# Kernel tuning notes

Measured on AMD Instinct MI355X. Metric: run time of the kernel, lower is better.

## Reference

```python
import jax, jax.numpy as jnp
import numpy as np
import math

BS, QL, KL = 2, 2048, 2048
H, D = 16, 64          # n_heads, cell_dim
QS = KS = VS = 1024    # query/key/value feature sizes
HD = H * D


def setup_inputs() -> dict:
    key = jax.random.key(0)
    ks = jax.random.split(key, 12)
    s_in = 1.0 / math.sqrt(QS)
    s_hd = 1.0 / math.sqrt(HD)
    return {
        "query": jax.random.normal(ks[0], (BS, QL, QS), jnp.float32),
        "key": jax.random.normal(ks[1], (BS, KL, KS), jnp.float32),
        "value": jax.random.normal(ks[2], (BS, KL, VS), jnp.float32),
        # nn.Linear weights stored as [in, out] for x @ W + b
        "Wq_w": jax.random.normal(ks[3], (QS, HD), jnp.float32) * s_in,
        "Wq_b": jax.random.normal(ks[4], (HD,), jnp.float32) * s_in,
        "Wk_w": jax.random.normal(ks[5], (KS, HD), jnp.float32) * s_in,
        "Wk_b": jax.random.normal(ks[6], (HD,), jnp.float32) * s_in,
        "Wv_w": jax.random.normal(ks[7], (VS, HD), jnp.float32) * s_in,
        "Wv_b": jax.random.normal(ks[8], (HD,), jnp.float32) * s_in,
        "Wo_w": jax.random.normal(ks[9], (HD, HD), jnp.float32) * s_hd,
        "Wo_b": jax.random.normal(ks[10], (HD,), jnp.float32) * s_hd,
    }


def reference(query, key, value, Wq_w, Wq_b, Wk_w, Wk_b, Wv_w, Wv_b, Wo_w, Wo_b):
    bs, ql, _ = query.shape
    kl = key.shape[1]
    # project and split heads; torch .chunk along dim 2 == head-major reshape
    q = (query @ Wq_w + Wq_b).reshape(bs, ql, H, D).transpose(0, 2, 1, 3)  # bhqd
    k = (key @ Wk_w + Wk_b).reshape(bs, kl, H, D).transpose(0, 2, 1, 3)    # bhkd
    v = (value @ Wv_w + Wv_b).reshape(bs, kl, H, D).transpose(0, 2, 1, 3)  # bhkd
    scores = jnp.einsum("bhqd,bhkd->bhqk", q, k) / jnp.sqrt(jnp.float32(D))
    # log_softmax(...).exp() == softmax (use_mask=False path)
    w = jax.nn.softmax(scores, axis=-1)
    heads = jnp.einsum("bhqk,bhkd->bhqd", w, v)
    out = heads.transpose(0, 2, 1, 3).reshape(bs, ql, HD)  # concat heads on dim 2
    return out @ Wo_w + Wo_b
```

## Files before the change

### kernel.cpp

```cpp
#include <hip/hip_runtime.h>

#define BSZ 2
#define SEQ 2048
#define NH 16
#define DHD 64
#define HDIM 1024
#define FS 1024
#define MR (BSZ*SEQ)
#define L2E 1.4426950408889634f

typedef __bf16 bf16x8 __attribute__((ext_vector_type(8)));
typedef __bf16 bf16x2t __attribute__((ext_vector_type(2)));
typedef float f32x4 __attribute__((ext_vector_type(4)));
typedef float f32x16 __attribute__((ext_vector_type(16)));
typedef unsigned short u16;
typedef unsigned int u32;

__device__ __forceinline__ u16 f2bf(float f) {
  u32 x = __float_as_uint(f);
  return (u16)((x + 0x7fffu + ((x >> 16) & 1u)) >> 16);
}

__device__ __forceinline__ u32 pack2bf(float a, float b) {
  bf16x2t t = {(__bf16)a, (__bf16)b};
  return __builtin_bit_cast(u32, t);
}

__device__ __forceinline__ void gload16(const void* g, void* l) {
  __builtin_amdgcn_global_load_lds(
      (const __attribute__((address_space(1))) u32*)g,
      (__attribute__((address_space(3))) u32*)l, 16, 0, 0);
}

__global__ __launch_bounds__(256) void cast3_k(const float* __restrict__ q,
                                               const float* __restrict__ k,
                                               const float* __restrict__ v,
                                               u16* __restrict__ dst, int n4) {
  int i = blockIdx.x * 256 + threadIdx.x;
  const int st = gridDim.x * 256;
  const int tot = 3 * n4;
  for (; i < tot; i += st) {
    const int arr = i >> 20;
    const int idx = i & (n4 - 1);
    const float* src = arr == 0 ? q : arr == 1 ? k : v;
    float4 vv = ((const float4*)src)[idx];
    ushort4 o;
    o.x = f2bf(vv.x); o.y = f2bf(vv.y); o.z = f2bf(vv.z); o.w = f2bf(vv.w);
    ((ushort4*)dst)[i] = o;
  }
}

__global__ __launch_bounds__(256) void transw4_k(
    const float* __restrict__ W0, const float* __restrict__ W1,
    const float* __restrict__ W2, const float* __restrict__ W3,
    u16* __restrict__ WTbase) {
  __shared__ float t[32][33];
  const int z = blockIdx.z;
  const float* W = z == 0 ? W0 : z == 1 ? W1 : z == 2 ? W2 : W3;
  u16* WT = WTbase + (size_t)z * FS * HDIM;
  const int tx = threadIdx.x, ty = threadIdx.y;
  const int c0 = blockIdx.x * 32, r0 = blockIdx.y * 32;
#pragma unroll
  for (int i = 0; i < 4; i++)
    t[ty + 8 * i][tx] = W[(size_t)(r0 + ty + 8 * i) * FS + c0 + tx];
  __syncthreads();
#pragma unroll
  for (int i = 0; i < 4; i++)
    WT[(size_t)(c0 + ty + 8 * i) * FS + r0 + tx] = f2bf(t[tx][ty + 8 * i]);
}

__global__ __launch_bounds__(256, 2) void gemmQKV_k(
    const u16* __restrict__ Abase, const u16* __restrict__ WTbase,
    const float* __restrict__ bq, const float* __restrict__ bk,
    const float* __restrict__ bv, u16* __restrict__ QKbase,
    u16* __restrict__ VpT) {
  __shared__ u16 aL[128 * 64];
  __shared__ u16 bL[128 * 64];
  const int grp = blockIdx.y;
  const u16* A = Abase + (size_t)grp * MR * FS;
  const u16* BT = WTbase + (size_t)grp * FS * HDIM;
  const float* bias = grp == 0 ? bq : grp == 1 ? bk : bv;
  const int m0 = (blockIdx.x >> 3) << 7;
  const int n0 = (blockIdx.x & 7) << 7;
  const int tid = threadIdx.x, w = tid >> 6, lane = tid & 63;
  const int wr = ((w >> 1) << 6), wc = ((w & 1) << 6);
  const int li = lane & 15, g = lane >> 4;

  f32x4 acc[4][4];
#pragma unroll
  for (int i = 0; i < 4; i++)
#pragma unroll
    for (int j = 0; j < 4; j++) acc[i][j] = (f32x4){0.f, 0.f, 0.f, 0.f};

  for (int k0 = 0; k0 < FS; k0 += 64) {
#pragma unroll
    for (int j = 0; j < 4; j++) {
      const int c = w * 4 + j;
      const int r = c * 8 + (lane >> 3);
      const int sc = (lane & 7) ^ (r & 7);
      gload16(A + (size_t)(m0 + r) * FS + k0 + sc * 8, (char*)aL + c * 1024);
      gload16(BT + (size_t)(n0 + r) * FS + k0 + sc * 8, (char*)bL + c * 1024);
    }
    __syncthreads();
    bf16x8 af[2][4], bfr[2][4];
#pragma unroll
    for (int ks = 0; ks < 2; ks++) {
#pragma unroll
      for (int mf = 0; mf < 4; mf++) {
        const int r = wr + mf * 16 + li;
        const int sl = (g + 4 * ks) ^ (r & 7);
        af[ks][mf] = *(const bf16x8*)((const char*)aL + r * 128 + sl * 16);
      }
#pragma unroll
      for (int nf = 0; nf < 4; nf++) {
        const int r = wc + nf * 16 + li;
        const int sl = (g + 4 * ks) ^ (r & 7);
        bfr[ks][nf] = *(const bf16x8*)((const char*)bL + r * 128 + sl * 16);
      }
    }
#pragma unroll
    for (int ks = 0; ks < 2; ks++)
#pragma unroll
      for (int mf = 0; mf < 4; mf++)
#pragma unroll
        for (int nf = 0; nf < 4; nf++)
          acc[mf][nf] = __builtin_amdgcn_mfma_f32_16x16x32_bf16(
              af[ks][mf], bfr[ks][nf], acc[mf][nf], 0, 0, 0);
    __syncthreads();
  }

  if (grp < 2) {
    const float osc = grp == 0 ? 0.125f * L2E : 1.0f;
    u16* C = QKbase + (size_t)grp * MR * HDIM;
#pragma unroll
    for (int mf = 0; mf < 4; mf++)
#pragma unroll
      for (int nf = 0; nf < 4; nf++) {
        const int n = n0 + wc + nf * 16 + li;
        const float bvl = bias[n];
#pragma unroll
        for (int r4 = 0; r4 < 4; r4++) {
          const int m = m0 + wr + mf * 16 + g * 4 + r4;
          C[(size_t)m * HDIM + n] = f2bf((acc[mf][nf][r4] + bvl) * osc);
        }
      }
  } else {
#pragma unroll
    for (int mf = 0; mf < 4; mf++)
#pragma unroll
      for (int nf = 0; nf < 4; nf++) {
        const int n = n0 + wc + nf * 16 + li;
        const float bvl = bias[n];
        const int m = m0 + wr + mf * 16 + g * 4;
        const int bb = m >> 11, kv = m & 2047;
        ushort4 o;
        o.x = f2bf(acc[mf][nf][0] + bvl);
        o.y = f2bf(acc[mf][nf][1] + bvl);
        o.z = f2bf(acc[mf][nf][2] + bvl);
        o.w = f2bf(acc[mf][nf][3] + bvl);
        *(ushort4*)(VpT +
                    ((size_t)(bb * NH + (n >> 6)) * DHD + (n & 63)) * SEQ + kv) = o;
      }
  }
}

__global__ __launch_bounds__(256, 2) void gemm_out_k(
    const u16* __restrict__ A, const u16* __restrict__ BT,
    const float* __restrict__ bias, float* __restrict__ C) {
  __shared__ u16 aL[128 * 64];
  __shared__ u16 bL[128 * 64];
  const int m0 = (blockIdx.x >> 3) << 7;
  const int n0 = (blockIdx.x & 7) << 7;
  const int tid = threadIdx.x, w = tid >> 6, lane = tid & 63;
  const int wr = ((w >> 1) << 6), wc = ((w & 1) << 6);
  const int li = lane & 15, g = lane >> 4;

  f32x4 acc[4][4];
#pragma unroll
  for (int i = 0; i < 4; i++)
#pragma unroll
    for (int j = 0; j < 4; j++) acc[i][j] = (f32x4){0.f, 0.f, 0.f, 0.f};

  for (int k0 = 0; k0 < HDIM; k0 += 64) {
#pragma unroll
    for (int j = 0; j < 4; j++) {
      const int c = w * 4 + j;
      const int r = c * 8 + (lane >> 3);
      const int sc = (lane & 7) ^ (r & 7);
      gload16(A + (size_t)(m0 + r) * HDIM + k0 + sc * 8, (char*)aL + c * 1024);
      gload16(BT + (size_t)(n0 + r) * HDIM + k0 + sc * 8, (char*)bL + c * 1024);
    }
    __syncthreads();
    bf16x8 af[2][4], bfr[2][4];
#pragma unroll
    for (int ks = 0; ks < 2; ks++) {
#pragma unroll
      for (int mf = 0; mf < 4; mf++) {
        const int r = wr + mf * 16 + li;
        const int sl = (g + 4 * ks) ^ (r & 7);
        af[ks][mf] = *(const bf16x8*)((const char*)aL + r * 128 + sl * 16);
      }
#pragma unroll
      for (int nf = 0; nf < 4; nf++) {
        const int r = wc + nf * 16 + li;
        const int sl = (g + 4 * ks) ^ (r & 7);
        bfr[ks][nf] = *(const bf16x8*)((const char*)bL + r * 128 + sl * 16);
      }
    }
#pragma unroll
    for (int ks = 0; ks < 2; ks++)
#pragma unroll
      for (int mf = 0; mf < 4; mf++)
#pragma unroll
        for (int nf = 0; nf < 4; nf++)
          acc[mf][nf] = __builtin_amdgcn_mfma_f32_16x16x32_bf16(
              af[ks][mf], bfr[ks][nf], acc[mf][nf], 0, 0, 0);
    __syncthreads();
  }

#pragma unroll
  for (int mf = 0; mf < 4; mf++)
#pragma unroll
    for (int nf = 0; nf < 4; nf++) {
      const int n = n0 + wc + nf * 16 + li;
      const float bvl = bias[n];
#pragma unroll
      for (int r4 = 0; r4 < 4; r4++) {
        const int m = m0 + wr + mf * 16 + g * 4 + r4;
        C[(size_t)m * HDIM + n] = acc[mf][nf][r4] + bvl;
      }
    }
}

__global__ __launch_bounds__(256, 2) void attn_k(
    const u16* __restrict__ Qp, const u16* __restrict__ Kp,
    const u16* __restrict__ VpT, u16* __restrict__ Hd) {
  __shared__ u16 kbuf[2][64 * 64];
  __shared__ u16 vbuf[2][64 * 64];
  __shared__ u16 pbuf[4][32 * 64];

  const int bid = blockIdx.x;
  const int swz = (bid & 7) * 64 + (bid >> 3);
  const int qb = swz & 15;
  const int h = (swz >> 4) & 15;
  const int b = swz >> 8;
  const int tid = threadIdx.x, w = tid >> 6, lane = tid & 63;
  const int q32 = lane & 31, hi = lane >> 5;
  const int q0 = qb << 7;
  const size_t qbase = (size_t)(b * SEQ + q0) * HDIM + (size_t)h * DHD;
  const size_t kbase = (size_t)(b * SEQ) * HDIM + (size_t)h * DHD;
  const size_t vtbase = (size_t)(b * NH + h) * DHD * SEQ;

  const int rr = lane >> 3;
  const int sc8 = ((lane & 7) ^ rr) * 8;

#pragma unroll
  for (int j = 0; j < 4; j++) {
    const int c = w * 4 + j;
    const int r = c * 8 + rr;
    gload16(Qp + qbase + (size_t)r * HDIM + sc8, (char*)kbuf + c * 1024);
  }
  __syncthreads();
  bf16x8 qf[4];
  {
    const int qrow = w * 32 + q32;
    const char* qbp = (const char*)kbuf + qrow * 128;
    const int qsw = (qrow & 7) << 4;
#pragma unroll
    for (int ds = 0; ds < 4; ds++)
      qf[ds] = *(const bf16x8*)(qbp + ((32 * ds + 16 * hi) ^ qsw));
  }
  __syncthreads();

  float mrun = -1e30f, lrun = 0.f;
  f32x16 o0, o1;
#pragma unroll
  for (int i = 0; i < 16; i++) { o0[i] = 0.f; o1[i] = 0.f; }

  char* pw = (char*)pbuf[w] + q32 * 128;
  const int psw = (q32 & 7) << 4;
  const int rsw = psw;

  auto stageKV = [&](int t, int buf) {
    const size_t kb = kbase + (size_t)(t * 64) * HDIM;
    const size_t vb = vtbase + (size_t)(t * 64);
#pragma unroll
    for (int j = 0; j < 2; j++) {
      const int c = w * 2 + j;
      const int r = c * 8 + rr;
      gload16(Kp + kb + (size_t)r * HDIM + sc8, (char*)kbuf[buf] + c * 1024);
      gload16(VpT + vb + (size_t)r * SEQ + sc8, (char*)vbuf[buf] + c * 1024);
    }
  };

  auto TILE = [&](int t, int par) {
    __syncthreads();
    if (t + 1 < SEQ / 64) stageKV(t + 1, par ^ 1);
    const char* kl = (const char*)kbuf[par];
    const char* vl = (const char*)vbuf[par];

    f32x16 s0, s1;
#pragma unroll
    for (int i = 0; i < 16; i++) { s0[i] = 0.f; s1[i] = 0.f; }
#pragma unroll
    for (int ds = 0; ds < 4; ds++) {
      const int off = (32 * ds + 16 * hi) ^ rsw;
      const bf16x8 ka = *(const bf16x8*)(kl + q32 * 128 + off);
      const bf16x8 kb2 = *(const bf16x8*)(kl + (32 + q32) * 128 + off);
      s0 = __builtin_amdgcn_mfma_f32_32x32x16_bf16(ka, qf[ds], s0, 0, 0, 0);
      s1 = __builtin_amdgcn_mfma_f32_32x32x16_bf16(kb2, qf[ds], s1, 0, 0, 0);
    }

    float mx = s0[0];
#pragma unroll
    for (int i = 1; i < 16; i++) mx = fmaxf(mx, s0[i]);
#pragma unroll
    for (int i = 0; i < 16; i++) mx = fmaxf(mx, s1[i]);
    mx = fmaxf(mx, __shfl_xor(mx, 32));
    if (!__all(mx <= mrun + 8.0f)) {
      const float mnew = fmaxf(mrun, mx);
      const float scl = __builtin_amdgcn_exp2f(mrun - mnew);
      mrun = mnew;
      lrun *= scl;
#pragma unroll
      for (int i = 0; i < 16; i++) { o0[i] *= scl; o1[i] *= scl; }
    }
    float p0[16], p1[16];
    float rs = 0.f;
#pragma unroll
    for (int i = 0; i < 16; i++) {
      p0[i] = __builtin_amdgcn_exp2f(s0[i] - mrun);
      p1[i] = __builtin_amdgcn_exp2f(s1[i] - mrun);
      rs += p0[i] + p1[i];
    }
    rs += __shfl_xor(rs, 32);
    lrun += rs;

#pragma unroll
    for (int rg = 0; rg < 4; rg++) {
      uint2 a2, b2;
      a2.x = pack2bf(p0[4 * rg + 0], p0[4 * rg + 1]);
      a2.y = pack2bf(p0[4 * rg + 2], p0[4 * rg + 3]);
      b2.x = pack2bf(p1[4 * rg + 0], p1[4 * rg + 1]);
      b2.y = pack2bf(p1[4 * rg + 2], p1[4 * rg + 3]);
      *(uint2*)(pw + ((16 * rg + 8 * hi) ^ psw)) = a2;
      *(uint2*)(pw + ((64 + 16 * rg + 8 * hi) ^ psw)) = b2;
    }

#pragma unroll
    for (int kvs = 0; kvs < 4; kvs++) {
      const int off = (32 * kvs + 16 * hi);
      const bf16x8 pf = *(const bf16x8*)(pw + (off ^ psw));
      const bf16x8 va = *(const bf16x8*)(vl + q32 * 128 + (off ^ rsw));
      const bf16x8 vb2 = *(const bf16x8*)(vl + (32 + q32) * 128 + (off ^ rsw));
      o0 = __builtin_amdgcn_mfma_f32_32x32x16_bf16(va, pf, o0, 0, 0, 0);
      o1 = __builtin_amdgcn_mfma_f32_32x32x16_bf16(vb2, pf, o1, 0, 0, 0);
    }
  };

  stageKV(0, 0);
#pragma unroll 1
  for (int tt = 0; tt < SEQ / 128; tt++) {
    TILE(2 * tt, 0);
    TILE(2 * tt + 1, 1);
  }

  const float inv = 1.f / lrun;
  const int q = q0 + w * 32 + q32;
  u16* orow = Hd + (size_t)(b * SEQ + q) * HDIM + (size_t)h * DHD;
#pragma unroll
  for (int rg = 0; rg < 4; rg++) {
    ushort4 ov;
    ov.x = f2bf(o0[4 * rg + 0] * inv);
    ov.y = f2bf(o0[4 * rg + 1] * inv);
    ov.z = f2bf(o0[4 * rg + 2] * inv);
    ov.w = f2bf(o0[4 * rg + 3] * inv);
    *(ushort4*)(orow + 8 * rg + 4 * hi) = ov;
    ushort4 ow;
    ow.x = f2bf(o1[4 * rg + 0] * inv);
    ow.y = f2bf(o1[4 * rg + 1] * inv);
    ow.z = f2bf(o1[4 * rg + 2] * inv);
    ow.w = f2bf(o1[4 * rg + 3] * inv);
    *(ushort4*)(orow + 32 + 8 * rg + 4 * hi) = ow;
  }
}

extern "C" void kernel_launch(void* const* d_in, const int* in_sizes, int n_in,
                              void* d_out, int out_size, void* d_ws, size_t ws_size,
                              hipStream_t stream) {
  (void)in_sizes; (void)n_in; (void)out_size; (void)ws_size;
  const float* q_in = (const float*)d_in[0];
  const float* k_in = (const float*)d_in[1];
  const float* v_in = (const float*)d_in[2];
  const float* Wq_w = (const float*)d_in[3];
  const float* Wq_b = (const float*)d_in[4];
  const float* Wk_w = (const float*)d_in[5];
  const float* Wk_b = (const float*)d_in[6];
  const float* Wv_w = (const float*)d_in[7];
  const float* Wv_b = (const float*)d_in[8];
  const float* Wo_w = (const float*)d_in[9];
  const float* Wo_b = (const float*)d_in[10];

  char* ws = (char*)d_ws;
  size_t off = 0;
  auto alloc = [&](size_t n) {
    char* p = ws + off;
    off += (n + 255) & ~(size_t)255;
    return p;
  };
  u16* qkv = (u16*)alloc((size_t)3 * MR * FS * 2);
  u16* wT = (u16*)alloc((size_t)4 * FS * HDIM * 2);
  u16* QK = (u16*)alloc((size_t)2 * MR * HDIM * 2);
  u16* VpT = (u16*)alloc((size_t)MR * HDIM * 2);
  u16* Hdp = (u16*)alloc((size_t)MR * HDIM * 2);

  const int n4 = MR * FS / 4;
  cast3_k<<<3072, 256, 0, stream>>>(q_in, k_in, v_in, qkv, n4);

  transw4_k<<<dim3(FS / 32, FS / 32, 4), dim3(32, 8), 0, stream>>>(
      Wq_w, Wk_w, Wv_w, Wo_w, wT);

  gemmQKV_k<<<dim3(256, 3), 256, 0, stream>>>(qkv, wT, Wq_b, Wk_b, Wv_b, QK,
                                              VpT);

  attn_k<<<BSZ * NH * (SEQ / 128), 256, 0, stream>>>(
      QK, QK + (size_t)MR * HDIM, VpT, Hdp);

  gemm_out_k<<<256, 256, 0, stream>>>(Hdp, wT + (size_t)3 * FS * HDIM, Wo_b,
                                      (float*)d_out);
}
```

Baseline: 133.4 us.

## Keep softmax P in registers via permlane swap and load V directly from global

New measurement: 149.3 us. 12.0% more time.

```diff
diff --git a/kernel.cpp b/kernel.cpp
--- a/kernel.cpp
+++ b/kernel.cpp
@@ -15,6 +15,7 @@
 typedef float f32x16 __attribute__((ext_vector_type(16)));
 typedef unsigned short u16;
 typedef unsigned int u32;
+typedef u32 u32x4 __attribute__((ext_vector_type(4)));
 
 __device__ __forceinline__ u16 f2bf(float f) {
   u32 x = __float_as_uint(f);
@@ -232,43 +233,42 @@
     }
 }
 
-__global__ __launch_bounds__(256, 2) void attn_k(
+__global__ __launch_bounds__(128, 2) void attn_k(
     const u16* __restrict__ Qp, const u16* __restrict__ Kp,
     const u16* __restrict__ VpT, u16* __restrict__ Hd) {
   __shared__ u16 kbuf[2][64 * 64];
-  __shared__ u16 vbuf[2][64 * 64];
-  __shared__ u16 pbuf[4][32 * 64];
 
   const int bid = blockIdx.x;
-  const int swz = (bid & 7) * 64 + (bid >> 3);
-  const int qb = swz & 15;
-  const int h = (swz >> 4) & 15;
-  const int b = swz >> 8;
+  const int swz = (bid & 7) * 128 + (bid >> 3);
+  const int qb = swz & 31;
+  const int h = (swz >> 5) & 15;
+  const int b = swz >> 9;
   const int tid = threadIdx.x, w = tid >> 6, lane = tid & 63;
   const int q32 = lane & 31, hi = lane >> 5;
-  const int q0 = qb << 7;
+  const int q0 = qb << 6;
   const size_t qbase = (size_t)(b * SEQ + q0) * HDIM + (size_t)h * DHD;
   const size_t kbase = (size_t)(b * SEQ) * HDIM + (size_t)h * DHD;
   const size_t vtbase = (size_t)(b * NH + h) * DHD * SEQ;
+  const u16* Vrow0 = VpT + vtbase + (size_t)q32 * SEQ + hi * 8;
+  const u16* Vrow1 = VpT + vtbase + (size_t)(32 + q32) * SEQ + hi * 8;
 
   const int rr = lane >> 3;
   const int sc8 = ((lane & 7) ^ rr) * 8;
+  const int fkey = (q32 & 7) << 4;
 
 #pragma unroll
   for (int j = 0; j < 4; j++) {
     const int c = w * 4 + j;
     const int r = c * 8 + rr;
-    gload16(Qp + qbase + (size_t)r * HDIM + sc8, (char*)kbuf + c * 1024);
+    gload16(Qp + qbase + (size_t)r * HDIM + sc8, (char*)kbuf[0] + c * 1024);
   }
   __syncthreads();
   bf16x8 qf[4];
   {
-    const int qrow = w * 32 + q32;
-    const char* qbp = (const char*)kbuf + qrow * 128;
-    const int qsw = (qrow & 7) << 4;
+    const char* qbp = (const char*)kbuf[0] + (w * 32 + q32) * 128;
 #pragma unroll
     for (int ds = 0; ds < 4; ds++)
-      qf[ds] = *(const bf16x8*)(qbp + ((32 * ds + 16 * hi) ^ qsw));
+      qf[ds] = *(const bf16x8*)(qbp + ((32 * ds + 16 * hi) ^ fkey));
   }
   __syncthreads();
 
@@ -277,45 +277,51 @@
 #pragma unroll
   for (int i = 0; i < 16; i++) { o0[i] = 0.f; o1[i] = 0.f; }
 
-  char* pw = (char*)pbuf[w] + q32 * 128;
-  const int psw = (q32 & 7) << 4;
-  const int rsw = psw;
-
-  auto stageKV = [&](int t, int buf) {
+  auto stageK = [&](int t, int buf) {
     const size_t kb = kbase + (size_t)(t * 64) * HDIM;
-    const size_t vb = vtbase + (size_t)(t * 64);
-#pragma unroll
-    for (int j = 0; j < 2; j++) {
-      const int c = w * 2 + j;
+#pragma unroll
+    for (int j = 0; j < 4; j++) {
+      const int c = w * 4 + j;
       const int r = c * 8 + rr;
       gload16(Kp + kb + (size_t)r * HDIM + sc8, (char*)kbuf[buf] + c * 1024);
-      gload16(VpT + vb + (size_t)r * SEQ + sc8, (char*)vbuf[buf] + c * 1024);
     }
   };
+
+  stageK(0, 0);
 
   auto TILE = [&](int t, int par) {
     __syncthreads();
-    if (t + 1 < SEQ / 64) stageKV(t + 1, par ^ 1);
+
+    bf16x8 vA0[4], vA1[4];
+    const int kvo = t * 64;
+#pragma unroll
+    for (int kvs = 0; kvs < 4; kvs++) {
+      vA0[kvs] = *(const bf16x8*)(Vrow0 + kvo + 16 * kvs);
+      vA1[kvs] = *(const bf16x8*)(Vrow1 + kvo + 16 * kvs);
+    }
+    if (t + 1 < SEQ / 64) stageK(t + 1, par ^ 1);
+
     const char* kl = (const char*)kbuf[par];
-    const char* vl = (const char*)vbuf[par];
-
     f32x16 s0, s1;
 #pragma unroll
     for (int i = 0; i < 16; i++) { s0[i] = 0.f; s1[i] = 0.f; }
 #pragma unroll
     for (int ds = 0; ds < 4; ds++) {
-      const int off = (32 * ds + 16 * hi) ^ rsw;
+      const int off = (32 * ds + 16 * hi) ^ fkey;
       const bf16x8 ka = *(const bf16x8*)(kl + q32 * 128 + off);
       const bf16x8 kb2 = *(const bf16x8*)(kl + (32 + q32) * 128 + off);
       s0 = __builtin_amdgcn_mfma_f32_32x32x16_bf16(ka, qf[ds], s0, 0, 0, 0);
       s1 = __builtin_amdgcn_mfma_f32_32x32x16_bf16(kb2, qf[ds], s1, 0, 0, 0);
     }
 
-    float mx = s0[0];
-#pragma unroll
-    for (int i = 1; i < 16; i++) mx = fmaxf(mx, s0[i]);
-#pragma unroll
-    for (int i = 0; i < 16; i++) mx = fmaxf(mx, s1[i]);
+    float mt[16];
+#pragma unroll
+    for (int i = 0; i < 16; i++) mt[i] = fmaxf(s0[i], s1[i]);
+#pragma unroll
+    for (int i = 0; i < 8; i++) mt[i] = fmaxf(mt[i], mt[i + 8]);
+#pragma unroll
+    for (int i = 0; i < 4; i++) mt[i] = fmaxf(mt[i], mt[i + 4]);
+    float mx = fmaxf(fmaxf(mt[0], mt[1]), fmaxf(mt[2], mt[3]));
     mx = fmaxf(mx, __shfl_xor(mx, 32));
     if (!__all(mx <= mrun + 8.0f)) {
       const float mnew = fmaxf(mrun, mx);
@@ -326,39 +332,39 @@
       for (int i = 0; i < 16; i++) { o0[i] *= scl; o1[i] *= scl; }
     }
     float p0[16], p1[16];
-    float rs = 0.f;
 #pragma unroll
     for (int i = 0; i < 16; i++) {
       p0[i] = __builtin_amdgcn_exp2f(s0[i] - mrun);
       p1[i] = __builtin_amdgcn_exp2f(s1[i] - mrun);
-      rs += p0[i] + p1[i];
-    }
+    }
+    float st[16];
+#pragma unroll
+    for (int i = 0; i < 16; i++) st[i] = p0[i] + p1[i];
+#pragma unroll
+    for (int i = 0; i < 8; i++) st[i] += st[i + 8];
+#pragma unroll
+    for (int i = 0; i < 4; i++) st[i] += st[i + 4];
+    float rs = (st[0] + st[1]) + (st[2] + st[3]);
     rs += __shfl_xor(rs, 32);
     lrun += rs;
 
 #pragma unroll
-    for (int rg = 0; rg < 4; rg++) {
-      uint2 a2, b2;
-      a2.x = pack2bf(p0[4 * rg + 0], p0[4 * rg + 1]);
-      a2.y = pack2bf(p0[4 * rg + 2], p0[4 * rg + 3]);
-      b2.x = pack2bf(p1[4 * rg + 0], p1[4 * rg + 1]);
-      b2.y = pack2bf(p1[4 * rg + 2], p1[4 * rg + 3]);
-      *(uint2*)(pw + ((16 * rg + 8 * hi) ^ psw)) = a2;
-      *(uint2*)(pw + ((64 + 16 * rg + 8 * hi) ^ psw)) = b2;
-    }
-
-#pragma unroll
     for (int kvs = 0; kvs < 4; kvs++) {
-      const int off = (32 * kvs + 16 * hi);
-      const bf16x8 pf = *(const bf16x8*)(pw + (off ^ psw));
-      const bf16x8 va = *(const bf16x8*)(vl + q32 * 128 + (off ^ rsw));
-      const bf16x8 vb2 = *(const bf16x8*)(vl + (32 + q32) * 128 + (off ^ rsw));
-      o0 = __builtin_amdgcn_mfma_f32_32x32x16_bf16(va, pf, o0, 0, 0, 0);
-      o1 = __builtin_amdgcn_mfma_f32_32x32x16_bf16(vb2, pf, o1, 0, 0, 0);
+      const float* ps = (kvs < 2) ? p0 : p1;
+      const int rb = (kvs & 1) * 8;
+      u32 w01 = pack2bf(ps[rb + 0], ps[rb + 1]);
+      u32 w23 = pack2bf(ps[rb + 2], ps[rb + 3]);
+      u32 w45 = pack2bf(ps[rb + 4], ps[rb + 5]);
+      u32 w67 = pack2bf(ps[rb + 6], ps[rb + 7]);
+      asm("v_permlane32_swap_b32 %0, %1" : "+v"(w01), "+v"(w45));
+      asm("v_permlane32_swap_b32 %0, %1" : "+v"(w23), "+v"(w67));
+      u32x4 uw = {w01, w23, w45, w67};
+      const bf16x8 pf = __builtin_bit_cast(bf16x8, uw);
+      o0 = __builtin_amdgcn_mfma_f32_32x32x16_bf16(vA0[kvs], pf, o0, 0, 0, 0);
+      o1 = __builtin_amdgcn_mfma_f32_32x32x16_bf16(vA1[kvs], pf, o1, 0, 0, 0);
     }
   };
 
-  stageKV(0, 0);
 #pragma unroll 1
   for (int tt = 0; tt < SEQ / 128; tt++) {
     TILE(2 * tt, 0);
@@ -423,7 +429,7 @@
   gemmQKV_k<<<dim3(256, 3), 256, 0, stream>>>(qkv, wT, Wq_b, Wk_b, Wv_b, QK,
                                               VpT);
 
-  attn_k<<<BSZ * NH * (SEQ / 128), 256, 0, stream>>>(
+  attn_k<<<BSZ * NH * (SEQ / 64), 128, 0, stream>>>(
       QK, QK + (size_t)MR * HDIM, VpT, Hdp);
 
   gemm_out_k<<<256, 256, 0, stream>>>(Hdp, wT + (size_t)3 * FS * HDIM, Wo_b,
```
